# Kernel tuning notes

Measured on AMD Instinct MI355X. Metric: run time of the kernel, lower is better.

## Reference

```python
import jax, jax.numpy as jnp
import numpy as np

N_HEADS = 16
HEAD_DIM = 128  # d_model // n_heads


def rope(x):
    # x: [B, H, T, D]. Matches the torch module: interleaved even/odd split,
    # then concat([x1*cos - x2*sin, x1*sin + x2*cos], axis=-1).
    T, D = x.shape[2], x.shape[3]
    inv_freq = 1.0 / (10000.0 ** (jnp.arange(0, D, 2, dtype=x.dtype) / D))  # [D/2]
    freqs = jnp.arange(T, dtype=x.dtype)[:, None] * inv_freq[None, :]       # [T, D/2]
    sin, cos = jnp.sin(freqs), jnp.cos(freqs)                               # [T, D/2]
    x1, x2 = x[..., ::2], x[..., 1::2]                                      # [B,H,T,D/2]
    return jnp.concatenate([x1 * cos - x2 * sin, x1 * sin + x2 * cos], axis=-1)


def setup_inputs() -> dict:
    key = jax.random.key(0)
    ks = jax.random.split(key, 5)
    B, T, C = 2, 2048, 2048
    scale = 1.0 / np.sqrt(C)
    return {
        "x": jax.random.normal(ks[0], (B, T, C), dtype=jnp.float32),
        "W_qkv": jax.random.normal(ks[1], (3 * C, C), dtype=jnp.float32) * scale,
        "b_qkv": jnp.zeros((3 * C,), dtype=jnp.float32),
        "W_out": jax.random.normal(ks[2], (C, C), dtype=jnp.float32) * scale,
        "b_out": jnp.zeros((C,), dtype=jnp.float32),
    }


def reference(x, W_qkv, b_qkv, W_out, b_out):
    B, T, C = x.shape
    H, D = N_HEADS, HEAD_DIM
    qkv = x @ W_qkv.T + b_qkv                      # [B, T, 3C]
    qkv = qkv.reshape(B, T, 3, H, D)
    q, k, v = qkv[:, :, 0], qkv[:, :, 1], qkv[:, :, 2]  # [B, T, H, D]
    q = rope(jnp.transpose(q, (0, 2, 1, 3)))       # [B, H, T, D]
    k = rope(jnp.transpose(k, (0, 2, 1, 3)))
    v = jnp.transpose(v, (0, 2, 1, 3))
    scores = jnp.einsum("bhqd,bhkd->bhqk", q, k) / jnp.sqrt(jnp.asarray(D, x.dtype))
    causal = jnp.tril(jnp.ones((T, T), dtype=bool))
    scores = jnp.where(causal, scores, jnp.finfo(x.dtype).min)
    attn = jax.nn.softmax(scores, axis=-1)
    out = jnp.einsum("bhqk,bhkd->bhqd", attn, v)   # [B, H, T, D]
    out = jnp.transpose(out, (0, 2, 1, 3)).reshape(B, T, C)
    return out @ W_out.T + b_out
```

## Files before the change

kernel.cpp:

```cpp
#include <hip/hip_runtime.h>
#include <hip/hip_bf16.h>

typedef __attribute__((ext_vector_type(8))) short bf16x8;
typedef __attribute__((ext_vector_type(4))) float f32x4;

#define GLOAD_LDS16(gptr, lptr) \
  __builtin_amdgcn_global_load_lds((const __attribute__((address_space(1))) void*)(gptr), \
                                   (__attribute__((address_space(3))) void*)(lptr), 16, 0, 0)

__device__ __forceinline__ unsigned short f2b(float f) {
  union { float f; unsigned u; } x; x.f = f;
  unsigned r = x.u + 0x7fffu + ((x.u >> 16) & 1u);
  return (unsigned short)(r >> 16);
}
__device__ __forceinline__ float b2f(unsigned short u) {
  union { unsigned u; float f; } x; x.u = ((unsigned)u) << 16;
  return x.f;
}
__device__ __forceinline__ unsigned cvt_pk_bf16(float lo, float hi) {
  unsigned d;
  asm("v_cvt_pk_bf16_f32 %0, %1, %2" : "=v"(d) : "v"(lo), "v"(hi));
  return d;
}

__global__ void cast3_kernel(const float* __restrict__ x,
                             const float* __restrict__ wq,
                             const float* __restrict__ wo,
                             unsigned short* __restrict__ out)
{
  const long n1 = 8388608L;
  const long n2 = 20971520L;
  const long i = ((long)blockIdx.x * 256 + threadIdx.x) * 4;
  const float* src; long off;
  if (i < n1)      { src = x;  off = i; }
  else if (i < n2) { src = wq; off = i - n1; }
  else             { src = wo; off = i - n2; }
  const float4 v = *(const float4*)(src + off);
  ushort4 r;
  r.x = f2b(v.x); r.y = f2b(v.y); r.z = f2b(v.z); r.w = f2b(v.w);
  *(ushort4*)(out + i) = r;
}

template<int MODE>
__global__ __launch_bounds__(512, 4)
void gemm128(const unsigned short* __restrict__ A,
             const unsigned short* __restrict__ Bm,
             const float* __restrict__ bias,
             void* __restrict__ Cp,
             unsigned short* __restrict__ Qr,
             unsigned short* __restrict__ Kr,
             unsigned short* __restrict__ Vr,
             int M, int N, int K)
{
  __shared__ __align__(16) char Lds[73728];
  const int t  = threadIdx.x;
  const int l  = t & 63;
  const int w  = t >> 6;
  const int lr = l & 15;
  const int lkb = (l >> 4) << 4;
  const int wr = w >> 2;
  const int wc = w & 3;

  const int nwg = gridDim.x;
  const int wg  = (blockIdx.x & 7) * (nwg >> 3) + (blockIdx.x >> 3);
  const int NBN = N >> 8;
  const int bm = wg / NBN, bn = wg % NBN;

  const long K2 = (long)K * 2;
  const char* Ab = (const char*)A  + (long)(bm * 128) * K2;
  const char* Bb = (const char*)Bm + (long)(bn * 256) * K2;

  auto swz = [](int a) -> int { return a ^ (((a >> 7) & 3) << 4); };

  const int t16 = t << 4;
  const int da  = swz(t16);
  const long sa = (long)(da >> 6) * K2 + (da & 63);
  const int db0 = swz(t16), db1 = swz(8192 + t16);
  const long sb0 = (long)(db0 >> 6) * K2 + (db0 & 63);
  const long sb1 = (long)(db1 >> 6) * K2 + (db1 & 63);

  auto stage = [&](int g) {
    char* S = Lds + (g % 3) * 24576;
    const char* As = Ab + (long)g * 64;
    const char* Bs = Bb + (long)g * 64;
    GLOAD_LDS16(As + sa,  S + t16);
    GLOAD_LDS16(Bs + sb0, S + 8192 + t16);
    GLOAD_LDS16(Bs + sb1, S + 16384 + t16);
  };

  int aoff[4], boff[4];
#pragma unroll
  for (int mi = 0; mi < 4; ++mi) {
    const int a = ((wr * 64 + mi * 16 + lr) << 6) | lkb;
    aoff[mi] = swz(a);
  }
#pragma unroll
  for (int ni = 0; ni < 4; ++ni) {
    const int a = ((wc * 64 + ni * 16 + lr) << 6) | lkb;
    boff[ni] = 8192 + swz(a);
  }

  f32x4 acc[4][4] = {};
  const int NT = K >> 5;
  bf16x8 af[4], bfr[4];

  stage(0); stage(1);
  asm volatile("s_waitcnt vmcnt(3)" ::: "memory");
  __builtin_amdgcn_s_barrier();
  __builtin_amdgcn_sched_barrier(0);
#pragma unroll
  for (int mi = 0; mi < 4; ++mi) af[mi]  = *(const bf16x8*)(Lds + aoff[mi]);
#pragma unroll
  for (int ni = 0; ni < 4; ++ni) bfr[ni] = *(const bf16x8*)(Lds + boff[ni]);

  for (int tt = 0; tt < NT; ++tt) {
    if (tt + 2 < NT) stage(tt + 2);
    __builtin_amdgcn_s_setprio(1);
#pragma unroll
    for (int mi = 0; mi < 4; ++mi)
#pragma unroll
      for (int ni = 0; ni < 4; ++ni)
        acc[mi][ni] = __builtin_amdgcn_mfma_f32_16x16x32_bf16(af[mi], bfr[ni], acc[mi][ni], 0, 0, 0);
    __builtin_amdgcn_s_setprio(0);
    if (tt + 1 < NT) {
      if (tt + 2 < NT) asm volatile("s_waitcnt vmcnt(3)" ::: "memory");
      else             asm volatile("s_waitcnt vmcnt(0)" ::: "memory");
      __builtin_amdgcn_s_barrier();
      __builtin_amdgcn_sched_barrier(0);
      const char* S = Lds + ((tt + 1) % 3) * 24576;
#pragma unroll
      for (int mi = 0; mi < 4; ++mi) af[mi]  = *(const bf16x8*)(S + aoff[mi]);
#pragma unroll
      for (int ni = 0; ni < 4; ++ni) bfr[ni] = *(const bf16x8*)(S + boff[ni]);
    }
  }

  const int roff = (l >> 4) << 2;
  const int row0 = bm * 128 + wr * 64 + roff;
  const int col0 = bn * 256 + wc * 64 + lr;
  float bv[4];
#pragma unroll
  for (int ni = 0; ni < 4; ++ni) bv[ni] = bias ? bias[col0 + ni * 16] : 0.0f;

  if (MODE == 1) {
#pragma unroll
    for (int mi = 0; mi < 4; ++mi) {
#pragma unroll
      for (int r = 0; r < 4; ++r) {
        const long rb = (long)(row0 + mi * 16 + r) * N;
#pragma unroll
        for (int ni = 0; ni < 4; ++ni)
          ((float*)Cp)[rb + col0 + ni * 16] = acc[mi][ni][r] + bv[ni];
      }
    }
  } else {
    const float C1 = 0.08838834764831845f * 1.4426950408889634f;
    const int sec = col0 >> 11;
    const int cq0 = col0 & 2047;
    const int parity = col0 & 1;
    int hh[4], dd[4], jj[4];
    float invf[4];
#pragma unroll
    for (int ni = 0; ni < 4; ++ni) {
      const int c = cq0 + ni * 16;
      hh[ni] = c >> 7;
      dd[ni] = c & 127;
      jj[ni] = dd[ni] >> 1;
      invf[ni] = exp2f(-(float)jj[ni] * 0.2076205059304602f);
    }
#pragma unroll
    for (int mi = 0; mi < 4; ++mi) {
#pragma unroll
      for (int r = 0; r < 4; ++r) {
        const int row = row0 + mi * 16 + r;
        const int b = row >> 11, tt = row & 2047;
#pragma unroll
        for (int ni = 0; ni < 4; ++ni) {
          const float val = acc[mi][ni][r] + bv[ni];
          if (sec == 2) {
            Vr[((long)((b << 4) | hh[ni]) * 2048 + tt) * 128 + dd[ni]] = f2b(val);
          } else {
            const float pv = __shfl_xor(val, 1, 64);
            float sn, cs;
            __sincosf((float)tt * invf[ni], &sn, &cs);
            float out = parity ? fmaf(pv, sn, val * cs) : fmaf(val, cs, -(pv * sn));
            const long addr = ((long)((b << 4) | hh[ni]) * 2048 + tt) * 128 + jj[ni] + (parity << 6);
            if (sec == 0) Qr[addr] = f2b(out);
            else          Kr[addr] = f2b(out * C1);
          }
        }
      }
    }
  }
}

__global__ void vtrans_kernel(const unsigned short* __restrict__ Vr,
                              unsigned short* __restrict__ Vt)
{
  __shared__ unsigned short ld[128][65];
  const int bh = blockIdx.y, tb = blockIdx.x;
  const int t = threadIdx.x;
#pragma unroll
  for (int i = 0; i < 32; ++i) {
    const int idx = i * 256 + t;
    const int d = idx & 127, tr = idx >> 7;
    ld[d][tr] = Vr[((long)bh * 2048 + tb * 64 + tr) * 128 + d];
  }
  __syncthreads();
#pragma unroll
  for (int i = 0; i < 32; ++i) {
    const int idx = i * 256 + t;
    const int tc = idx & 63, dr = idx >> 6;
    Vt[((long)bh * 128 + dr) * 2048 + tb * 64 + tc] = ld[dr][tc];
  }
}

__global__ __launch_bounds__(256)
void attn_fwd(const unsigned short* __restrict__ Q,
              const unsigned short* __restrict__ Kg,
              const unsigned short* __restrict__ Vt,
              unsigned short* __restrict__ O, int T)
{
  __shared__ __align__(16) unsigned short Ks[2][64 * 128];
  __shared__ __align__(16) unsigned short Vs[128 * 64];
  const int t = threadIdx.x;
  const int w = t >> 6, l = t & 63;
  const int lr = l & 15;
  const int g  = l >> 4;
  const int g16 = g << 4;
  const int sw = (lr & 7) << 4;
  const int bh = blockIdx.x;
  const int qt = (gridDim.y - 1) - blockIdx.y;
  const int q0 = qt * 64 + w * 16;
  const long hbase = (long)bh * T * 128;
  const long hbase2 = hbase * 2;
  const long T2 = (long)T * 2;
  const int roff = g << 2;

  bf16x8 qf[4];
  const unsigned short* Qrow = Q + hbase + (long)(q0 + lr) * 128;
#pragma unroll
  for (int ds = 0; ds < 4; ++ds) qf[ds] = *(const bf16x8*)&Qrow[ds * 32 + (g16 >> 1)];

  f32x4 o[8] = {};
  float m = -INFINITY, lsum = 0.f;

  auto stageK = [&](int kt, int buf) {
#pragma unroll
    for (int c = 0; c < 4; ++c) {
      const int o2 = t * 16 + c * 4096;
      const int krow = o2 >> 8, kcb = o2 & 255;
      GLOAD_LDS16((const char*)Kg + hbase2 + (long)kt * 16384 + krow * 256 + (kcb ^ ((krow & 7) << 4)),
                  (char*)Ks[buf] + o2);
    }
  };
  auto stageV = [&](int kt) {
#pragma unroll
    for (int c = 0; c < 4; ++c) {
      const int o2 = t * 16 + c * 4096;
      const int vrow = o2 >> 7, vcb = o2 & 127;
      GLOAD_LDS16((const char*)Vt + (long)(bh * 128 + vrow) * T2 + (long)kt * 128 + (vcb ^ ((vrow & 7) << 4)),
                  (char*)Vs + o2);
    }
  };

  const int ntile = qt + 1;
  stageK(0, 0);
  stageV(0);
  __syncthreads();

  for (int kt = 0; kt < ntile; ++kt) {
    const int cur = kt & 1;
    if (kt + 1 < ntile) stageK(kt + 1, cur ^ 1);

    const char* KsB = (const char*)Ks[cur];

    f32x4 s[4] = {};
    __builtin_amdgcn_s_setprio(1);
#pragma unroll
    for (int tj = 0; tj < 4; ++tj)
#pragma unroll
      for (int ds = 0; ds < 4; ++ds) {
        bf16x8 kf = *(const bf16x8*)(KsB + (tj * 16 + lr) * 256 + ((ds * 64 + g16) ^ sw));
        s[tj] = __builtin_amdgcn_mfma_f32_16x16x32_bf16(kf, qf[ds], s[tj], 0, 0, 0);
      }
    __builtin_amdgcn_s_setprio(0);

    if (kt == qt) {
#pragma unroll
      for (int tj = 0; tj < 4; ++tj)
#pragma unroll
        for (int r = 0; r < 4; ++r)
          if (kt * 64 + tj * 16 + 4 * g + r > q0 + lr) s[tj][r] = -INFINITY;
    }

    float pmax = -INFINITY;
#pragma unroll
    for (int tj = 0; tj < 4; ++tj)
#pragma unroll
      for (int r = 0; r < 4; ++r) pmax = fmaxf(pmax, s[tj][r]);
    pmax = fmaxf(pmax, __shfl_xor(pmax, 16, 64));
    pmax = fmaxf(pmax, __shfl_xor(pmax, 32, 64));

    const bool need = !__all(pmax - m <= 8.0f);
    float corr = 1.0f;
    if (need) {
      const float mn = fmaxf(m, pmax);
      corr = exp2f(m - mn);
      m = mn;
    }

    float p[4][4];
    float rs = 0.f;
#pragma unroll
    for (int tj = 0; tj < 4; ++tj)
#pragma unroll
      for (int r = 0; r < 4; ++r) {
        const float pv = exp2f(s[tj][r] - m);
        p[tj][r] = pv;
        rs += pv;
      }
    rs += __shfl_xor(rs, 16, 64);
    rs += __shfl_xor(rs, 32, 64);
    lsum = lsum * corr + rs;

    unsigned D8[4][2];
#pragma unroll
    for (int tj = 0; tj < 4; ++tj) {
      D8[tj][0] = cvt_pk_bf16(p[tj][0], p[tj][1]);
      D8[tj][1] = cvt_pk_bf16(p[tj][2], p[tj][3]);
    }

    if (need) {
      float corrj[4];
#pragma unroll
      for (int j = 0; j < 4; ++j) corrj[j] = __shfl(corr, roff + j, 64);
#pragma unroll
      for (int nj = 0; nj < 8; ++nj)
#pragma unroll
        for (int j = 0; j < 4; ++j) o[nj][j] *= corrj[j];
    }

    if (kt + 1 < ntile) asm volatile("s_waitcnt vmcnt(4)" ::: "memory");
    else                asm volatile("s_waitcnt vmcnt(0)" ::: "memory");
    __builtin_amdgcn_s_barrier();
    __builtin_amdgcn_sched_barrier(0);

    __builtin_amdgcn_s_setprio(1);
#pragma unroll
    for (int ks = 0; ks < 2; ++ks) {
      union { unsigned u[4]; bf16x8 v; } pfu;
#pragma unroll
      for (int k2 = 0; k2 < 4; ++k2) {
        const int src = lr | ((2 * (g & 1) + (k2 >> 1)) << 4);
        const unsigned dwA = __shfl(D8[2 * ks][k2 & 1], src, 64);
        const unsigned dwB = __shfl(D8[2 * ks + 1][k2 & 1], src, 64);
        pfu.u[k2] = (g & 2) ? dwB : dwA;
      }
#pragma unroll
      for (int nj = 0; nj < 8; ++nj) {
        bf16x8 vf = *(const bf16x8*)((const char*)Vs + (nj * 16 + lr) * 128 + ((ks * 64 + g16) ^ sw));
        o[nj] = __builtin_amdgcn_mfma_f32_16x16x32_bf16(pfu.v, vf, o[nj], 0, 0, 0);
      }
    }
    __builtin_amdgcn_s_setprio(0);

    __syncthreads();
    if (kt + 1 < ntile) stageV(kt + 1);
  }

  const float inv = 1.0f / lsum;
  float invj[4];
#pragma unroll
  for (int j = 0; j < 4; ++j) invj[j] = __shfl(inv, roff + j, 64);
  const int b = bh >> 4, h = bh & 15;
#pragma unroll
  for (int nj = 0; nj < 8; ++nj)
#pragma unroll
    for (int j = 0; j < 4; ++j) {
      const int q = q0 + roff + j;
      const int d = nj * 16 + lr;
      O[(long)(b * T + q) * 2048 + h * 128 + d] = f2b(o[nj][j] * invj[j]);
    }
}

extern "C" void kernel_launch(void* const* d_in, const int* in_sizes, int n_in,
                              void* d_out, int out_size, void* d_ws, size_t ws_size,
                              hipStream_t stream)
{
  const int B = 2, T = 2048, C = 2048;
  const int M = B * T;
  const int N1 = 3 * C;
  const float* x    = (const float*)d_in[0];
  const float* Wqkv = (const float*)d_in[1];
  const float* bqkv = (const float*)d_in[2];
  const float* Wout = (const float*)d_in[3];
  const float* bout = (const float*)d_in[4];
  float* out = (float*)d_out;

  char* p = (char*)d_ws;
  unsigned short* xb    = (unsigned short*)p; p += (size_t)M * C * 2;
  unsigned short* wqkvb = (unsigned short*)p; p += (size_t)N1 * C * 2;
  unsigned short* woutb = (unsigned short*)p; p += (size_t)C * C * 2;
  unsigned short* Vr    = (unsigned short*)p; p += (size_t)M * C * 2;
  unsigned short* Qr    = (unsigned short*)p; p += (size_t)M * C * 2;
  unsigned short* Kr    = (unsigned short*)p; p += (size_t)M * C * 2;
  unsigned short* Vt    = (unsigned short*)p; p += (size_t)M * C * 2;
  unsigned short* Ob    = xb;

  const long ncast = (long)M * C + (long)N1 * C + (long)C * C;
  cast3_kernel<<<(int)(ncast / 1024), 256, 0, stream>>>(x, Wqkv, Wout, xb);

  gemm128<2><<<dim3((M / 128) * (N1 / 256)), 512, 0, stream>>>(
      xb, wqkvb, bqkv, nullptr, Qr, Kr, Vr, M, N1, C);

  vtrans_kernel<<<dim3(T / 64, 32), 256, 0, stream>>>(Vr, Vt);

  attn_fwd<<<dim3(32, T / 64), 256, 0, stream>>>(Qr, Kr, Vt, Ob, T);

  gemm128<1><<<dim3((M / 128) * (C / 256)), 512, 0, stream>>>(
      Ob, woutb, bout, out, nullptr, nullptr, nullptr, M, C, C);
}
```

Baseline: 281.6 us.

## Write V transposed from QKV GEMM epilogue and use precomputed RoPE table

```diff
diff --git a/kernel.cpp b/kernel.cpp
--- a/kernel.cpp
+++ b/kernel.cpp
@@ -26,19 +26,31 @@
 __global__ void cast3_kernel(const float* __restrict__ x,
                              const float* __restrict__ wq,
                              const float* __restrict__ wo,
-                             unsigned short* __restrict__ out)
+                             unsigned short* __restrict__ out,
+                             float2* __restrict__ tab)
 {
   const long n1 = 8388608L;
   const long n2 = 20971520L;
-  const long i = ((long)blockIdx.x * 256 + threadIdx.x) * 4;
-  const float* src; long off;
-  if (i < n1)      { src = x;  off = i; }
-  else if (i < n2) { src = wq; off = i - n1; }
-  else             { src = wo; off = i - n2; }
-  const float4 v = *(const float4*)(src + off);
-  ushort4 r;
-  r.x = f2b(v.x); r.y = f2b(v.y); r.z = f2b(v.z); r.w = f2b(v.w);
-  *(ushort4*)(out + i) = r;
+  const long nc = 25165824L;
+  const long tid = (long)blockIdx.x * 256 + threadIdx.x;
+  const long i = tid * 4;
+  if (i < nc) {
+    const float* src; long off;
+    if (i < n1)      { src = x;  off = i; }
+    else if (i < n2) { src = wq; off = i - n1; }
+    else             { src = wo; off = i - n2; }
+    const float4 v = *(const float4*)(src + off);
+    ushort4 r;
+    r.x = f2b(v.x); r.y = f2b(v.y); r.z = f2b(v.z); r.w = f2b(v.w);
+    *(ushort4*)(out + i) = r;
+  } else {
+    const int k = (int)(tid - nc / 4);
+    const int tt = k >> 6, j = k & 63;
+    const float inv = exp2f(-(float)j * 0.2076205059304602f);
+    float sn, cs;
+    sincosf((float)tt * inv, &sn, &cs);
+    tab[k] = make_float2(cs, sn);
+  }
 }
 
 template<int MODE>
@@ -49,7 +61,8 @@
              void* __restrict__ Cp,
              unsigned short* __restrict__ Qr,
              unsigned short* __restrict__ Kr,
-             unsigned short* __restrict__ Vr,
+             unsigned short* __restrict__ Vt,
+             const float2* __restrict__ tab,
              int M, int N, int K)
 {
   __shared__ __align__(16) char Lds[73728];
@@ -159,59 +172,49 @@
     const int cq0 = col0 & 2047;
     const int parity = col0 & 1;
     int hh[4], dd[4], jj[4];
-    float invf[4];
 #pragma unroll
     for (int ni = 0; ni < 4; ++ni) {
       const int c = cq0 + ni * 16;
       hh[ni] = c >> 7;
       dd[ni] = c & 127;
       jj[ni] = dd[ni] >> 1;
-      invf[ni] = exp2f(-(float)jj[ni] * 0.2076205059304602f);
-    }
-#pragma unroll
-    for (int mi = 0; mi < 4; ++mi) {
-#pragma unroll
-      for (int r = 0; r < 4; ++r) {
-        const int row = row0 + mi * 16 + r;
-        const int b = row >> 11, tt = row & 2047;
+    }
+    if (sec == 2) {
+#pragma unroll
+      for (int mi = 0; mi < 4; ++mi) {
+        const int tt0 = row0 + mi * 16;
+        const int b = tt0 >> 11, ttl = tt0 & 2047;
 #pragma unroll
         for (int ni = 0; ni < 4; ++ni) {
-          const float val = acc[mi][ni][r] + bv[ni];
-          if (sec == 2) {
-            Vr[((long)((b << 4) | hh[ni]) * 2048 + tt) * 128 + dd[ni]] = f2b(val);
-          } else {
+          ushort4 pk;
+          pk.x = f2b(acc[mi][ni][0] + bv[ni]);
+          pk.y = f2b(acc[mi][ni][1] + bv[ni]);
+          pk.z = f2b(acc[mi][ni][2] + bv[ni]);
+          pk.w = f2b(acc[mi][ni][3] + bv[ni]);
+          *(ushort4*)&Vt[((long)((b << 4) | hh[ni]) * 128 + dd[ni]) * 2048 + ttl] = pk;
+        }
+      }
+    } else {
+#pragma unroll
+      for (int mi = 0; mi < 4; ++mi) {
+#pragma unroll
+        for (int r = 0; r < 4; ++r) {
+          const int row = row0 + mi * 16 + r;
+          const int b = row >> 11, tt = row & 2047;
+#pragma unroll
+          for (int ni = 0; ni < 4; ++ni) {
+            const float val = acc[mi][ni][r] + bv[ni];
             const float pv = __shfl_xor(val, 1, 64);
-            float sn, cs;
-            __sincosf((float)tt * invf[ni], &sn, &cs);
-            float out = parity ? fmaf(pv, sn, val * cs) : fmaf(val, cs, -(pv * sn));
+            const float2 t2 = tab[tt * 64 + jj[ni]];
+            const float outv = parity ? fmaf(pv, t2.y, val * t2.x)
+                                      : fmaf(val, t2.x, -(pv * t2.y));
             const long addr = ((long)((b << 4) | hh[ni]) * 2048 + tt) * 128 + jj[ni] + (parity << 6);
-            if (sec == 0) Qr[addr] = f2b(out);
-            else          Kr[addr] = f2b(out * C1);
+            if (sec == 0) Qr[addr] = f2b(outv);
+            else          Kr[addr] = f2b(outv * C1);
           }
         }
       }
     }
-  }
-}
-
-__global__ void vtrans_kernel(const unsigned short* __restrict__ Vr,
-                              unsigned short* __restrict__ Vt)
-{
-  __shared__ unsigned short ld[128][65];
-  const int bh = blockIdx.y, tb = blockIdx.x;
-  const int t = threadIdx.x;
-#pragma unroll
-  for (int i = 0; i < 32; ++i) {
-    const int idx = i * 256 + t;
-    const int d = idx & 127, tr = idx >> 7;
-    ld[d][tr] = Vr[((long)bh * 2048 + tb * 64 + tr) * 128 + d];
-  }
-  __syncthreads();
-#pragma unroll
-  for (int i = 0; i < 32; ++i) {
-    const int idx = i * 256 + t;
-    const int tc = idx & 63, dr = idx >> 6;
-    Vt[((long)bh * 128 + dr) * 2048 + tb * 64 + tc] = ld[dr][tc];
   }
 }
 
@@ -402,22 +405,19 @@
   unsigned short* xb    = (unsigned short*)p; p += (size_t)M * C * 2;
   unsigned short* wqkvb = (unsigned short*)p; p += (size_t)N1 * C * 2;
   unsigned short* woutb = (unsigned short*)p; p += (size_t)C * C * 2;
-  unsigned short* Vr    = (unsigned short*)p; p += (size_t)M * C * 2;
   unsigned short* Qr    = (unsigned short*)p; p += (size_t)M * C * 2;
   unsigned short* Kr    = (unsigned short*)p; p += (size_t)M * C * 2;
   unsigned short* Vt    = (unsigned short*)p; p += (size_t)M * C * 2;
+  float2*         tab   = (float2*)p;         p += (size_t)T * 64 * sizeof(float2);
   unsigned short* Ob    = xb;
 
-  const long ncast = (long)M * C + (long)N1 * C + (long)C * C;
-  cast3_kernel<<<(int)(ncast / 1024), 256, 0, stream>>>(x, Wqkv, Wout, xb);
+  cast3_kernel<<<24576 + 512, 256, 0, stream>>>(x, Wqkv, Wout, xb, tab);
 
   gemm128<2><<<dim3((M / 128) * (N1 / 256)), 512, 0, stream>>>(
-      xb, wqkvb, bqkv, nullptr, Qr, Kr, Vr, M, N1, C);
-
-  vtrans_kernel<<<dim3(T / 64, 32), 256, 0, stream>>>(Vr, Vt);
+      xb, wqkvb, bqkv, nullptr, Qr, Kr, Vt, tab, M, N1, C);
 
   attn_fwd<<<dim3(32, T / 64), 256, 0, stream>>>(Qr, Kr, Vt, Ob, T);
 
   gemm128<1><<<dim3((M / 128) * (C / 256)), 512, 0, stream>>>(
-      Ob, woutb, bout, out, nullptr, nullptr, nullptr, M, C, C);
-}
+      Ob, woutb, bout, out, nullptr, nullptr, nullptr, nullptr, M, C, C);
+}
```

Measured after the change: 272.4 us, median of 2. 3.3% less time.
